# Kernel tuning notes

Measured on AMD Instinct MI355X. Metric: run time of the kernel, lower is better.

The kernel has to match this reference:

```python
import jax, jax.numpy as jnp
import numpy as np

EPS = 1e-5


def setup_inputs() -> dict:
    key = jax.random.key(0)
    ks = jax.random.split(key, 14)
    N, C, H, W, D = 2048, 512, 4, 4, 64
    inp = {
        "x": jax.random.normal(ks[0], (N, C, H, W), jnp.float32),
        "W123": jax.random.normal(ks[1], (3, D, C), jnp.float32) * 0.05,
        "b123": jax.random.normal(ks[2], (3, D), jnp.float32) * 0.05,
        "g123": jax.random.uniform(ks[3], (3, D), jnp.float32, 0.5, 1.5),
        "be123": jax.random.normal(ks[4], (3, D), jnp.float32) * 0.05,
        "m123": jax.random.normal(ks[5], (3, D), jnp.float32) * 0.05,
        "v123": jax.random.uniform(ks[6], (3, D), jnp.float32, 0.5, 1.5),
        "W4": jax.random.normal(ks[7], (C, D), jnp.float32) * 0.05,
        "b4": jax.random.normal(ks[8], (C,), jnp.float32) * 0.05,
        "g4": jax.random.uniform(ks[9], (C,), jnp.float32, 0.5, 1.5),
        "be4": jax.random.normal(ks[10], (C,), jnp.float32) * 0.05,
        "m4": jax.random.normal(ks[11], (C,), jnp.float32) * 0.05,
        "v4": jax.random.uniform(ks[12], (C,), jnp.float32, 0.5, 1.5),
    }
    return inp


def reference(x, W123, b123, g123, be123, m123, v123, W4, b4, g4, be4, m4, v4):
    N, C, H, W = x.shape
    D = W123.shape[1]
    # three parallel 1x1 stride-2 conv branches == strided slice + channel GEMM
    xs = x[:, :, ::2, ::2]                                 # (N, C, H/2, W/2)
    proj = jnp.einsum('nchw,koc->knohw', xs, W123)         # (3, N, D, H/2, W/2)
    bcast = lambda p: p[:, None, :, None, None]
    bn = (proj + bcast(b123) - bcast(m123)) * (bcast(g123) / jnp.sqrt(bcast(v123) + EPS)) + bcast(be123)
    act = jax.nn.relu(bn)                                  # (3, N, D, h, w)
    L = act.shape[-2] * act.shape[-1]
    q = act[0].reshape(N, D, L).transpose(0, 2, 1)         # (N, L, D)
    k = act[1].reshape(N, D, L)                            # (N, D, L)
    v = act[2].reshape(N, D, L).transpose(0, 2, 1)         # (N, L, D)
    attn = jax.nn.softmax(jnp.einsum('nld,ndm->nlm', q, k), axis=2)  # (N, L, L)
    att = jnp.einsum('nlm,nmd->nld', attn, v).transpose(0, 2, 1)     # (N, D, L)
    att = att.reshape(N, D, W, -1)                         # (N, D, W, L//W)
    # conv2: 1x1 conv D->C + BN (no ReLU)
    out2 = jnp.einsum('ndhw,cd->nchw', att, W4) + b4[None, :, None, None]
    cb = lambda p: p[None, :, None, None]
    bn2 = (out2 - cb(m4)) * (cb(g4) / jnp.sqrt(cb(v4) + EPS)) + cb(be4)
    return x + bn2                                         # broadcasts (N,C,4,1) -> (N,C,4,4)
```

## Files before the change

### kernel.cpp

```cpp
#include <hip/hip_runtime.h>
#include <hip/hip_bf16.h>
#include <math.h>

#define EPS 1e-5f

typedef __attribute__((ext_vector_type(8))) short bf8_t;
typedef __attribute__((ext_vector_type(4))) float f4_t;

static __device__ __forceinline__ unsigned short f2b(float f) {
    __hip_bfloat16 h = __float2bfloat16(f);
    return *reinterpret_cast<unsigned short*>(&h);
}


__global__ __launch_bounds__(256) void k0_prep(
    const float* __restrict__ W123, const float* __restrict__ W4,
    const float* __restrict__ b123, const float* __restrict__ g123,
    const float* __restrict__ be123, const float* __restrict__ m123, const float* __restrict__ v123,
    const float* __restrict__ b4, const float* __restrict__ g4,
    const float* __restrict__ be4, const float* __restrict__ m4, const float* __restrict__ v4,
    unsigned short* __restrict__ w1b, unsigned short* __restrict__ w4b,
    float* __restrict__ bn1s, float* __restrict__ bn1h,
    float* __restrict__ bn2s, float* __restrict__ bn2h)
{
    const int bid = blockIdx.x, tid = threadIdx.x;
    if (bid == 64) {
        if (tid < 192) {
            float s = g123[tid] * rsqrtf(v123[tid] + EPS);
            bn1s[tid] = s;
            bn1h[tid] = be123[tid] + (b123[tid] - m123[tid]) * s;
        }
        for (int c = tid; c < 512; c += 256) {
            float s = g4[c] * rsqrtf(v4[c] + EPS);
            bn2s[c] = s;
            bn2h[c] = be4[c] + (b4[c] - m4[c]) * s;
        }
        return;
    }
    const int f = bid * 256 + tid;
    const float* src;
    unsigned short* dst;
    if (f < 12288) {
        int mt = f >> 10, ks = (f >> 6) & 15, lane = f & 63;
        int row = mt * 16 + (lane & 15);
        int k0  = ks * 32 + ((lane >> 4) << 3);
        src = W123 + row * 512 + k0;
        dst = w1b + f * 8;
    } else {
        int f2 = f - 12288;
        int mt = f2 >> 7, ks = (f2 >> 6) & 1, lane = f2 & 63;
        int row = mt * 16 + (lane & 15);
        int k0  = ks * 32 + ((lane >> 4) << 3);
        src = W4 + row * 64 + k0;
        dst = w4b + f2 * 8;
    }
    float4 a = *(const float4*)src;
    float4 b = *(const float4*)(src + 4);
    union { unsigned short u[8]; uint4 v; } o;
    o.u[0]=f2b(a.x); o.u[1]=f2b(a.y); o.u[2]=f2b(a.z); o.u[3]=f2b(a.w);
    o.u[4]=f2b(b.x); o.u[5]=f2b(b.y); o.u[6]=f2b(b.z); o.u[7]=f2b(b.w);
    *(uint4*)dst = o.v;
}

__global__ __launch_bounds__(256) void k1_mfma(
    const float* __restrict__ x,
    const unsigned short* __restrict__ w1b,
    const unsigned short* __restrict__ w4b,
    const float* __restrict__ bn1s, const float* __restrict__ bn1h,
    const float* __restrict__ bn2s, const float* __restrict__ bn2h,
    float* __restrict__ out)
{
    __shared__ unsigned short Bxs[16][536];
    __shared__ float actL[192][17];
    __shared__ float smx[4][17];
    __shared__ unsigned short B2[16][72];

    const int tid = threadIdx.x;
    const int lane = tid & 63, w = tid >> 6;
    const int n0 = blockIdx.x * 4;

    #pragma unroll
    for (int it = 0; it < 8; ++it) {
        int i = it * 256 + tid;
        int s = i >> 9, c = i & 511;
        const float* xp = x + (size_t)(n0 + s) * 8192 + c * 16;
        float4 a = *(const float4*)xp;
        float4 b = *(const float4*)(xp + 8);
        Bxs[s * 4 + 0][c] = f2b(a.x);
        Bxs[s * 4 + 1][c] = f2b(a.z);
        Bxs[s * 4 + 2][c] = f2b(b.x);
        Bxs[s * 4 + 3][c] = f2b(b.z);
    }
    __syncthreads();

    {
        f4_t acc[3] = {};
        const bf8_t* Af = (const bf8_t*)w1b;
        const int col = lane & 15, kg = (lane >> 4) << 3;
        for (int ks = 0; ks < 16; ++ks) {
            bf8_t bf = *(const bf8_t*)&Bxs[col][ks * 32 + kg];
            #pragma unroll
            for (int mi = 0; mi < 3; ++mi) {
                int mt = w * 3 + mi;
                bf8_t af = Af[(mt * 16 + ks) * 64 + lane];
                acc[mi] = __builtin_amdgcn_mfma_f32_16x16x32_bf16(af, bf, acc[mi], 0, 0, 0);
            }
        }
        #pragma unroll
        for (int mi = 0; mi < 3; ++mi) {
            int rbase = (w * 3 + mi) * 16 + ((lane >> 4) << 2);
            #pragma unroll
            for (int r = 0; r < 4; ++r) {
                int row = rbase + r;
                float v = acc[mi][r] * bn1s[row] + bn1h[row];
                actL[row][col] = fmaxf(v, 0.f);
            }
        }
    }
    __syncthreads();

    if (tid < 128) {
        int s = tid >> 5, l = (tid >> 3) & 3, m = (tid >> 1) & 3, dg = tid & 1;
        float part = 0.f;
        #pragma unroll 8
        for (int k = 0; k < 32; ++k) {
            int d = dg * 32 + k;
            part += actL[d][s * 4 + l] * actL[64 + d][s * 4 + m];
        }
        part += __shfl_xor(part, 1);
        if (dg == 0) smx[s][l * 4 + m] = part;
    }
    __syncthreads();

    if (tid < 16) {
        int s = tid >> 2, l = tid & 3;
        float s0 = smx[s][l*4+0], s1 = smx[s][l*4+1], s2 = smx[s][l*4+2], s3 = smx[s][l*4+3];
        float mx = fmaxf(fmaxf(s0, s1), fmaxf(s2, s3));
        float e0 = expf(s0-mx), e1 = expf(s1-mx), e2 = expf(s2-mx), e3 = expf(s3-mx);
        float inv = 1.f / (e0 + e1 + e2 + e3);
        smx[s][l*4+0] = e0*inv; smx[s][l*4+1] = e1*inv;
        smx[s][l*4+2] = e2*inv; smx[s][l*4+3] = e3*inv;
    }
    __syncthreads();

    if (tid < 128) {
        int s = tid >> 5, l = (tid >> 3) & 3, d0 = (tid & 7) * 8;
        float p0 = smx[s][l*4+0], p1 = smx[s][l*4+1], p2 = smx[s][l*4+2], p3 = smx[s][l*4+3];
        #pragma unroll
        for (int j = 0; j < 8; ++j) {
            int d = d0 + j;
            float sum = p0 * actL[128+d][s*4+0] + p1 * actL[128+d][s*4+1]
                      + p2 * actL[128+d][s*4+2] + p3 * actL[128+d][s*4+3];
            B2[s * 4 + l][d] = f2b(sum);
        }
    }
    __syncthreads();

    {
        const bf8_t* A2f = (const bf8_t*)w4b;
        const int col = lane & 15, kg = (lane >> 4) << 3;
        f4_t acc2[8] = {};
        #pragma unroll
        for (int ks = 0; ks < 2; ++ks) {
            bf8_t bf = *(const bf8_t*)&B2[col][ks * 32 + kg];
            #pragma unroll
            for (int mi = 0; mi < 8; ++mi) {
                int mt = w * 8 + mi;
                bf8_t af = A2f[(mt * 2 + ks) * 64 + lane];
                acc2[mi] = __builtin_amdgcn_mfma_f32_16x16x32_bf16(af, bf, acc2[mi], 0, 0, 0);
            }
        }
        const int s = col >> 2, l = col & 3;
        const float* xn = x + (size_t)(n0 + s) * 8192 + l * 4;
        float* on = out + (size_t)(n0 + s) * 8192 + l * 4;
        #pragma unroll
        for (int mi = 0; mi < 8; ++mi) {
            int cbase = (w * 8 + mi) * 16 + ((lane >> 4) << 2);
            #pragma unroll
            for (int r = 0; r < 4; ++r) {
                int c = cbase + r;
                float b = acc2[mi][r] * bn2s[c] + bn2h[c];
                float4 xv = *(const float4*)(xn + c * 16);
                *(float4*)(on + c * 16) = make_float4(xv.x + b, xv.y + b, xv.z + b, xv.w + b);
            }
        }
    }
}

extern "C" void kernel_launch(void* const* d_in, const int* in_sizes, int n_in,
                              void* d_out, int out_size, void* d_ws, size_t ws_size,
                              hipStream_t stream) {
    const float* x     = (const float*)d_in[0];
    const float* W123  = (const float*)d_in[1];
    const float* b123  = (const float*)d_in[2];
    const float* g123  = (const float*)d_in[3];
    const float* be123 = (const float*)d_in[4];
    const float* m123  = (const float*)d_in[5];
    const float* v123  = (const float*)d_in[6];
    const float* W4    = (const float*)d_in[7];
    const float* b4    = (const float*)d_in[8];
    const float* g4    = (const float*)d_in[9];
    const float* be4   = (const float*)d_in[10];
    const float* m4    = (const float*)d_in[11];
    const float* v4    = (const float*)d_in[12];
    float* outp = (float*)d_out;

    char* ws = (char*)d_ws;
    unsigned short* w1b = (unsigned short*)ws;
    unsigned short* w4b = (unsigned short*)(ws + 196608);
    float* bn1s = (float*)(ws + 262144);
    float* bn1h = (float*)(ws + 262912);
    float* bn2s = (float*)(ws + 263680);
    float* bn2h = (float*)(ws + 265728);

    k0_prep<<<65, 256, 0, stream>>>(W123, W4, b123, g123, be123, m123, v123,
                                    b4, g4, be4, m4, v4,
                                    w1b, w4b, bn1s, bn1h, bn2s, bn2h);
    k1_mfma<<<512, 256, 0, stream>>>(x, w1b, w4b, bn1s, bn1h, bn2s, bn2h, outp);
}
```

Baseline: 152.6 us.

## Halve samples per block and stage epilogue through LDS for coalesced stores

Each block now handles 2 samples instead of 4, doubling the grid to 1024 blocks for better CU occupancy and latency hiding. The 16-column MFMA tiles are half-filled, with columns duplicated via col&7, so half the matrix-core work is wasted. The final residual add now writes the BN2 results to a shared transpose buffer and then streams x and out with contiguous float4 accesses per thread, replacing the scattered 16-float-stride epilogue. Each block also re-reads the weights for fewer samples, which raises total weight traffic.

```diff
diff --git a/kernel.cpp b/kernel.cpp
--- a/kernel.cpp
+++ b/kernel.cpp
@@ -70,17 +70,18 @@
     const float* __restrict__ bn2s, const float* __restrict__ bn2h,
     float* __restrict__ out)
 {
-    __shared__ unsigned short Bxs[16][536];
-    __shared__ float actL[192][17];
-    __shared__ float smx[4][17];
-    __shared__ unsigned short B2[16][72];
+    __shared__ unsigned short Bxs[8][536];
+    __shared__ float actL[192][9];
+    __shared__ float smx[2][17];
+    __shared__ unsigned short B2[8][72];
+    __shared__ float C2T[8][524];
 
     const int tid = threadIdx.x;
     const int lane = tid & 63, w = tid >> 6;
-    const int n0 = blockIdx.x * 4;
+    const int n0 = blockIdx.x * 2;
 
     #pragma unroll
-    for (int it = 0; it < 8; ++it) {
+    for (int it = 0; it < 4; ++it) {
         int i = it * 256 + tid;
         int s = i >> 9, c = i & 511;
         const float* xp = x + (size_t)(n0 + s) * 8192 + c * 16;
@@ -98,7 +99,7 @@
         const bf8_t* Af = (const bf8_t*)w1b;
         const int col = lane & 15, kg = (lane >> 4) << 3;
         for (int ks = 0; ks < 16; ++ks) {
-            bf8_t bf = *(const bf8_t*)&Bxs[col][ks * 32 + kg];
+            bf8_t bf = *(const bf8_t*)&Bxs[col & 7][ks * 32 + kg];
             #pragma unroll
             for (int mi = 0; mi < 3; ++mi) {
                 int mt = w * 3 + mi;
@@ -106,20 +107,22 @@
                 acc[mi] = __builtin_amdgcn_mfma_f32_16x16x32_bf16(af, bf, acc[mi], 0, 0, 0);
             }
         }
-        #pragma unroll
-        for (int mi = 0; mi < 3; ++mi) {
-            int rbase = (w * 3 + mi) * 16 + ((lane >> 4) << 2);
-            #pragma unroll
-            for (int r = 0; r < 4; ++r) {
-                int row = rbase + r;
-                float v = acc[mi][r] * bn1s[row] + bn1h[row];
-                actL[row][col] = fmaxf(v, 0.f);
-            }
-        }
-    }
-    __syncthreads();
-
-    if (tid < 128) {
+        if (col < 8) {
+            #pragma unroll
+            for (int mi = 0; mi < 3; ++mi) {
+                int rbase = (w * 3 + mi) * 16 + ((lane >> 4) << 2);
+                #pragma unroll
+                for (int r = 0; r < 4; ++r) {
+                    int row = rbase + r;
+                    float v = acc[mi][r] * bn1s[row] + bn1h[row];
+                    actL[row][col] = fmaxf(v, 0.f);
+                }
+            }
+        }
+    }
+    __syncthreads();
+
+    if (tid < 64) {
         int s = tid >> 5, l = (tid >> 3) & 3, m = (tid >> 1) & 3, dg = tid & 1;
         float part = 0.f;
         #pragma unroll 8
@@ -132,7 +135,7 @@
     }
     __syncthreads();
 
-    if (tid < 16) {
+    if (tid < 8) {
         int s = tid >> 2, l = tid & 3;
         float s0 = smx[s][l*4+0], s1 = smx[s][l*4+1], s2 = smx[s][l*4+2], s3 = smx[s][l*4+3];
         float mx = fmaxf(fmaxf(s0, s1), fmaxf(s2, s3));
@@ -143,7 +146,7 @@
     }
     __syncthreads();
 
-    if (tid < 128) {
+    if (tid < 64) {
         int s = tid >> 5, l = (tid >> 3) & 3, d0 = (tid & 7) * 8;
         float p0 = smx[s][l*4+0], p1 = smx[s][l*4+1], p2 = smx[s][l*4+2], p3 = smx[s][l*4+3];
         #pragma unroll
@@ -162,7 +165,7 @@
         f4_t acc2[8] = {};
         #pragma unroll
         for (int ks = 0; ks < 2; ++ks) {
-            bf8_t bf = *(const bf8_t*)&B2[col][ks * 32 + kg];
+            bf8_t bf = *(const bf8_t*)&B2[col & 7][ks * 32 + kg];
             #pragma unroll
             for (int mi = 0; mi < 8; ++mi) {
                 int mt = w * 8 + mi;
@@ -170,20 +173,32 @@
                 acc2[mi] = __builtin_amdgcn_mfma_f32_16x16x32_bf16(af, bf, acc2[mi], 0, 0, 0);
             }
         }
-        const int s = col >> 2, l = col & 3;
-        const float* xn = x + (size_t)(n0 + s) * 8192 + l * 4;
-        float* on = out + (size_t)(n0 + s) * 8192 + l * 4;
-        #pragma unroll
-        for (int mi = 0; mi < 8; ++mi) {
-            int cbase = (w * 8 + mi) * 16 + ((lane >> 4) << 2);
-            #pragma unroll
-            for (int r = 0; r < 4; ++r) {
-                int c = cbase + r;
-                float b = acc2[mi][r] * bn2s[c] + bn2h[c];
-                float4 xv = *(const float4*)(xn + c * 16);
-                *(float4*)(on + c * 16) = make_float4(xv.x + b, xv.y + b, xv.z + b, xv.w + b);
-            }
-        }
+        if (col < 8) {
+            #pragma unroll
+            for (int mi = 0; mi < 8; ++mi) {
+                int cbase = (w * 8 + mi) * 16 + ((lane >> 4) << 2);
+                #pragma unroll
+                for (int r = 0; r < 4; ++r) {
+                    int c = cbase + r;
+                    C2T[col][c] = acc2[mi][r] * bn2s[c] + bn2h[c];
+                }
+            }
+        }
+    }
+    __syncthreads();
+
+    #pragma unroll
+    for (int it = 0; it < 8; ++it) {
+        int j = it * 256 + tid;
+        int s = j >> 10, rem = j & 1023, c = rem >> 1, half = rem & 1;
+        const float* xp = x + (size_t)(n0 + s) * 8192 + c * 16 + half * 8;
+        float* op = out + (size_t)(n0 + s) * 8192 + c * 16 + half * 8;
+        float b0 = C2T[s * 4 + half * 2 + 0][c];
+        float b1 = C2T[s * 4 + half * 2 + 1][c];
+        float4 x0 = *(const float4*)xp;
+        float4 x1 = *(const float4*)(xp + 4);
+        *(float4*)op       = make_float4(x0.x + b0, x0.y + b0, x0.z + b0, x0.w + b0);
+        *(float4*)(op + 4) = make_float4(x1.x + b1, x1.y + b1, x1.z + b1, x1.w + b1);
     }
 }
 
@@ -216,5 +231,5 @@
     k0_prep<<<65, 256, 0, stream>>>(W123, W4, b123, g123, be123, m123, v123,
                                     b4, g4, be4, m4, v4,
                                     w1b, w4b, bn1s, bn1h, bn2s, bn2h);
-    k1_mfma<<<512, 256, 0, stream>>>(x, w1b, w4b, bn1s, bn1h, bn2s, bn2h, outp);
-}
+    k1_mfma<<<1024, 256, 0, stream>>>(x, w1b, w4b, bn1s, bn1h, bn2s, bn2h, outp);
+}
```

Result: no change. 152.1 us (-0.4%).

## Process one sample per block with shrunk aliased LDS and coalesced x I/O

Applied to the files above, without the earlier changes.

Switches from four samples per block to one sample per block, quadrupling the grid, and overlays the LDS buffers to cut shared memory so more blocks fit per CU. Input x is now read with fully coalesced float4 loads. The residual output is staged through LDS and written coalesced. In exchange, the 16-wide MFMA column dimension is mostly wasted and each block re-reads the full bf16 weight tiles, raising total weight traffic fourfold.

```diff
diff --git a/kernel.cpp b/kernel.cpp
--- a/kernel.cpp
+++ b/kernel.cpp
@@ -62,7 +62,7 @@
     *(uint4*)dst = o.v;
 }
 
-__global__ __launch_bounds__(256) void k1_mfma(
+__global__ __launch_bounds__(256, 8) void k1_mfma(
     const float* __restrict__ x,
     const unsigned short* __restrict__ w1b,
     const unsigned short* __restrict__ w4b,
@@ -70,35 +70,41 @@
     const float* __restrict__ bn2s, const float* __restrict__ bn2h,
     float* __restrict__ out)
 {
-    __shared__ unsigned short Bxs[16][536];
-    __shared__ float actL[192][17];
-    __shared__ float smx[4][17];
-    __shared__ unsigned short B2[16][72];
+    __shared__ __align__(16) char U[8768];
+    __shared__ float smx[20];
+
+    unsigned short* Bxs  = (unsigned short*)&U[0];
+    float*          actL = (float*)&U[4160];
+    unsigned short* B2   = (unsigned short*)&U[0];
+    float*          bn2L = (float*)&U[576];
 
     const int tid = threadIdx.x;
     const int lane = tid & 63, w = tid >> 6;
-    const int n0 = blockIdx.x * 4;
+    const int n = blockIdx.x;
+    const float4* x4 = (const float4*)(x + (size_t)n * 8192);
+    float4* o4 = (float4*)(out + (size_t)n * 8192);
 
     #pragma unroll
-    for (int it = 0; it < 8; ++it) {
-        int i = it * 256 + tid;
-        int s = i >> 9, c = i & 511;
-        const float* xp = x + (size_t)(n0 + s) * 8192 + c * 16;
-        float4 a = *(const float4*)xp;
-        float4 b = *(const float4*)(xp + 8);
-        Bxs[s * 4 + 0][c] = f2b(a.x);
-        Bxs[s * 4 + 1][c] = f2b(a.z);
-        Bxs[s * 4 + 2][c] = f2b(b.x);
-        Bxs[s * 4 + 3][c] = f2b(b.z);
+    for (int k = 0; k < 8; ++k) {
+        int f = tid + k * 256;
+        float4 v = x4[f];
+        int c = f >> 2, j = f & 3;
+        if (j == 0) {
+            Bxs[0 * 520 + c] = f2b(v.x);
+            Bxs[1 * 520 + c] = f2b(v.z);
+        } else if (j == 2) {
+            Bxs[2 * 520 + c] = f2b(v.x);
+            Bxs[3 * 520 + c] = f2b(v.z);
+        }
     }
     __syncthreads();
 
     {
         f4_t acc[3] = {};
         const bf8_t* Af = (const bf8_t*)w1b;
-        const int col = lane & 15, kg = (lane >> 4) << 3;
+        const int col = lane & 15, kb = (lane >> 4) << 3;
         for (int ks = 0; ks < 16; ++ks) {
-            bf8_t bf = *(const bf8_t*)&Bxs[col][ks * 32 + kg];
+            bf8_t bf = *(const bf8_t*)&Bxs[(col & 3) * 520 + ks * 32 + kb];
             #pragma unroll
             for (int mi = 0; mi < 3; ++mi) {
                 int mt = w * 3 + mi;
@@ -106,63 +112,65 @@
                 acc[mi] = __builtin_amdgcn_mfma_f32_16x16x32_bf16(af, bf, acc[mi], 0, 0, 0);
             }
         }
-        #pragma unroll
-        for (int mi = 0; mi < 3; ++mi) {
-            int rbase = (w * 3 + mi) * 16 + ((lane >> 4) << 2);
-            #pragma unroll
-            for (int r = 0; r < 4; ++r) {
-                int row = rbase + r;
-                float v = acc[mi][r] * bn1s[row] + bn1h[row];
-                actL[row][col] = fmaxf(v, 0.f);
-            }
-        }
-    }
-    __syncthreads();
-
-    if (tid < 128) {
-        int s = tid >> 5, l = (tid >> 3) & 3, m = (tid >> 1) & 3, dg = tid & 1;
+        if (col < 4) {
+            #pragma unroll
+            for (int mi = 0; mi < 3; ++mi) {
+                int rbase = (w * 3 + mi) * 16 + ((lane >> 4) << 2);
+                #pragma unroll
+                for (int r = 0; r < 4; ++r) {
+                    int row = rbase + r;
+                    float v = acc[mi][r] * bn1s[row] + bn1h[row];
+                    actL[row * 5 + col] = fmaxf(v, 0.f);
+                }
+            }
+        }
+    }
+    __syncthreads();
+
+    if (tid < 32) {
+        int l = (tid >> 3) & 3, m = (tid >> 1) & 3, dg = tid & 1;
         float part = 0.f;
         #pragma unroll 8
-        for (int k = 0; k < 32; ++k) {
-            int d = dg * 32 + k;
-            part += actL[d][s * 4 + l] * actL[64 + d][s * 4 + m];
+        for (int kk = 0; kk < 32; ++kk) {
+            int d = dg * 32 + kk;
+            part += actL[d * 5 + l] * actL[(64 + d) * 5 + m];
         }
         part += __shfl_xor(part, 1);
-        if (dg == 0) smx[s][l * 4 + m] = part;
-    }
-    __syncthreads();
-
-    if (tid < 16) {
-        int s = tid >> 2, l = tid & 3;
-        float s0 = smx[s][l*4+0], s1 = smx[s][l*4+1], s2 = smx[s][l*4+2], s3 = smx[s][l*4+3];
+        if (dg == 0) smx[l * 4 + m] = part;
+    }
+    __syncthreads();
+
+    if (tid < 4) {
+        int l = tid;
+        float s0 = smx[l*4+0], s1 = smx[l*4+1], s2 = smx[l*4+2], s3 = smx[l*4+3];
         float mx = fmaxf(fmaxf(s0, s1), fmaxf(s2, s3));
         float e0 = expf(s0-mx), e1 = expf(s1-mx), e2 = expf(s2-mx), e3 = expf(s3-mx);
         float inv = 1.f / (e0 + e1 + e2 + e3);
-        smx[s][l*4+0] = e0*inv; smx[s][l*4+1] = e1*inv;
-        smx[s][l*4+2] = e2*inv; smx[s][l*4+3] = e3*inv;
-    }
-    __syncthreads();
-
-    if (tid < 128) {
-        int s = tid >> 5, l = (tid >> 3) & 3, d0 = (tid & 7) * 8;
-        float p0 = smx[s][l*4+0], p1 = smx[s][l*4+1], p2 = smx[s][l*4+2], p3 = smx[s][l*4+3];
+        smx[l*4+0] = e0*inv; smx[l*4+1] = e1*inv;
+        smx[l*4+2] = e2*inv; smx[l*4+3] = e3*inv;
+    }
+    __syncthreads();
+
+    if (tid < 32) {
+        int l = tid >> 3, d0 = (tid & 7) * 8;
+        float p0 = smx[l*4+0], p1 = smx[l*4+1], p2 = smx[l*4+2], p3 = smx[l*4+3];
         #pragma unroll
         for (int j = 0; j < 8; ++j) {
             int d = d0 + j;
-            float sum = p0 * actL[128+d][s*4+0] + p1 * actL[128+d][s*4+1]
-                      + p2 * actL[128+d][s*4+2] + p3 * actL[128+d][s*4+3];
-            B2[s * 4 + l][d] = f2b(sum);
+            float sum = p0 * actL[(128+d)*5 + 0] + p1 * actL[(128+d)*5 + 1]
+                      + p2 * actL[(128+d)*5 + 2] + p3 * actL[(128+d)*5 + 3];
+            B2[l * 72 + d] = f2b(sum);
         }
     }
     __syncthreads();
 
     {
         const bf8_t* A2f = (const bf8_t*)w4b;
-        const int col = lane & 15, kg = (lane >> 4) << 3;
+        const int col = lane & 15, kb = (lane >> 4) << 3;
         f4_t acc2[8] = {};
         #pragma unroll
         for (int ks = 0; ks < 2; ++ks) {
-            bf8_t bf = *(const bf8_t*)&B2[col][ks * 32 + kg];
+            bf8_t bf = *(const bf8_t*)&B2[(col & 3) * 72 + ks * 32 + kb];
             #pragma unroll
             for (int mi = 0; mi < 8; ++mi) {
                 int mt = w * 8 + mi;
@@ -170,20 +178,27 @@
                 acc2[mi] = __builtin_amdgcn_mfma_f32_16x16x32_bf16(af, bf, acc2[mi], 0, 0, 0);
             }
         }
-        const int s = col >> 2, l = col & 3;
-        const float* xn = x + (size_t)(n0 + s) * 8192 + l * 4;
-        float* on = out + (size_t)(n0 + s) * 8192 + l * 4;
-        #pragma unroll
-        for (int mi = 0; mi < 8; ++mi) {
-            int cbase = (w * 8 + mi) * 16 + ((lane >> 4) << 2);
-            #pragma unroll
-            for (int r = 0; r < 4; ++r) {
-                int c = cbase + r;
-                float b = acc2[mi][r] * bn2s[c] + bn2h[c];
-                float4 xv = *(const float4*)(xn + c * 16);
-                *(float4*)(on + c * 16) = make_float4(xv.x + b, xv.y + b, xv.z + b, xv.w + b);
-            }
-        }
+        if (col < 4) {
+            #pragma unroll
+            for (int mi = 0; mi < 8; ++mi) {
+                int cbase = (w * 8 + mi) * 16 + ((lane >> 4) << 2);
+                #pragma unroll
+                for (int r = 0; r < 4; ++r) {
+                    int c = cbase + r;
+                    bn2L[c * 4 + col] = acc2[mi][r] * bn2s[c] + bn2h[c];
+                }
+            }
+        }
+    }
+    __syncthreads();
+
+    #pragma unroll
+    for (int k = 0; k < 8; ++k) {
+        int f = tid + k * 256;
+        int c = f >> 2, j = f & 3;
+        float b = bn2L[c * 4 + j];
+        float4 v = x4[f];
+        o4[f] = make_float4(v.x + b, v.y + b, v.z + b, v.w + b);
     }
 }
 
@@ -216,5 +231,5 @@
     k0_prep<<<65, 256, 0, stream>>>(W123, W4, b123, g123, be123, m123, v123,
                                     b4, g4, be4, m4, v4,
                                     w1b, w4b, bn1s, bn1h, bn2s, bn2h);
-    k1_mfma<<<512, 256, 0, stream>>>(x, w1b, w4b, bn1s, bn1h, bn2s, bn2h, outp);
-}
+    k1_mfma<<<2048, 256, 0, stream>>>(x, w1b, w4b, bn1s, bn1h, bn2s, bn2h, outp);
+}
```

New measurement: 188.1 us. 23.2% more time.

## Split fused kernel into attention and output kernels with coalesced epilogue

Applied to the files above, without the earlier changes.

Splits the single fused kernel in two. The first computes the attention output and writes it to a bf16 workspace; the second, launched one block per sample, applies the output projection and residual add, staging BN results in shared memory so x is read and out is written as fully coalesced float4 streams. The first kernel also hoists its global x loads ahead of the LDS stores and software-prefetches the weight fragments two k-steps ahead in the MFMA loop. The cost is an extra launch, a workspace round trip, and a second full read of x, in exchange for better memory access patterns and higher parallelism in the output stage.

```diff
diff --git a/kernel.cpp b/kernel.cpp
--- a/kernel.cpp
+++ b/kernel.cpp
@@ -62,34 +62,36 @@
     *(uint4*)dst = o.v;
 }
 
-__global__ __launch_bounds__(256) void k1_mfma(
+__global__ __launch_bounds__(256) void k1_att(
     const float* __restrict__ x,
     const unsigned short* __restrict__ w1b,
-    const unsigned short* __restrict__ w4b,
     const float* __restrict__ bn1s, const float* __restrict__ bn1h,
-    const float* __restrict__ bn2s, const float* __restrict__ bn2h,
-    float* __restrict__ out)
+    unsigned short* __restrict__ attg)
 {
     __shared__ unsigned short Bxs[16][536];
     __shared__ float actL[192][17];
     __shared__ float smx[4][17];
-    __shared__ unsigned short B2[16][72];
 
     const int tid = threadIdx.x;
     const int lane = tid & 63, w = tid >> 6;
     const int n0 = blockIdx.x * 4;
 
+    float4 xa[8], xb[8];
+    #pragma unroll
+    for (int it = 0; it < 8; ++it) {
+        int i = it * 256 + tid;
+        const float* xp = x + (size_t)(n0 + (i >> 9)) * 8192 + (i & 511) * 16;
+        xa[it] = *(const float4*)xp;
+        xb[it] = *(const float4*)(xp + 8);
+    }
     #pragma unroll
     for (int it = 0; it < 8; ++it) {
         int i = it * 256 + tid;
         int s = i >> 9, c = i & 511;
-        const float* xp = x + (size_t)(n0 + s) * 8192 + c * 16;
-        float4 a = *(const float4*)xp;
-        float4 b = *(const float4*)(xp + 8);
-        Bxs[s * 4 + 0][c] = f2b(a.x);
-        Bxs[s * 4 + 1][c] = f2b(a.z);
-        Bxs[s * 4 + 2][c] = f2b(b.x);
-        Bxs[s * 4 + 3][c] = f2b(b.z);
+        Bxs[s * 4 + 0][c] = f2b(xa[it].x);
+        Bxs[s * 4 + 1][c] = f2b(xa[it].z);
+        Bxs[s * 4 + 2][c] = f2b(xb[it].x);
+        Bxs[s * 4 + 3][c] = f2b(xb[it].z);
     }
     __syncthreads();
 
@@ -97,14 +99,23 @@
         f4_t acc[3] = {};
         const bf8_t* Af = (const bf8_t*)w1b;
         const int col = lane & 15, kg = (lane >> 4) << 3;
+        bf8_t afp[3][3];
+        #pragma unroll
+        for (int mi = 0; mi < 3; ++mi) {
+            afp[0][mi] = Af[((w * 3 + mi) * 16 + 0) * 64 + lane];
+            afp[1][mi] = Af[((w * 3 + mi) * 16 + 1) * 64 + lane];
+        }
+        #pragma unroll
         for (int ks = 0; ks < 16; ++ks) {
+            if (ks < 14) {
+                #pragma unroll
+                for (int mi = 0; mi < 3; ++mi)
+                    afp[(ks + 2) % 3][mi] = Af[((w * 3 + mi) * 16 + ks + 2) * 64 + lane];
+            }
             bf8_t bf = *(const bf8_t*)&Bxs[col][ks * 32 + kg];
             #pragma unroll
-            for (int mi = 0; mi < 3; ++mi) {
-                int mt = w * 3 + mi;
-                bf8_t af = Af[(mt * 16 + ks) * 64 + lane];
-                acc[mi] = __builtin_amdgcn_mfma_f32_16x16x32_bf16(af, bf, acc[mi], 0, 0, 0);
-            }
+            for (int mi = 0; mi < 3; ++mi)
+                acc[mi] = __builtin_amdgcn_mfma_f32_16x16x32_bf16(afp[ks % 3][mi], bf, acc[mi], 0, 0, 0);
         }
         #pragma unroll
         for (int mi = 0; mi < 3; ++mi) {
@@ -146,23 +157,52 @@
     if (tid < 128) {
         int s = tid >> 5, l = (tid >> 3) & 3, d0 = (tid & 7) * 8;
         float p0 = smx[s][l*4+0], p1 = smx[s][l*4+1], p2 = smx[s][l*4+2], p3 = smx[s][l*4+3];
+        union { unsigned short u[8]; uint4 v; } o;
         #pragma unroll
         for (int j = 0; j < 8; ++j) {
             int d = d0 + j;
             float sum = p0 * actL[128+d][s*4+0] + p1 * actL[128+d][s*4+1]
                       + p2 * actL[128+d][s*4+2] + p3 * actL[128+d][s*4+3];
-            B2[s * 4 + l][d] = f2b(sum);
-        }
+            o.u[j] = f2b(sum);
+        }
+        *(uint4*)&attg[(size_t)(n0 + s) * 256 + l * 64 + d0] = o.v;
+    }
+}
+
+__global__ __launch_bounds__(256) void k2_out(
+    const float* __restrict__ x,
+    const unsigned short* __restrict__ attg,
+    const unsigned short* __restrict__ w4b,
+    const float* __restrict__ bn2s, const float* __restrict__ bn2h,
+    float* __restrict__ out)
+{
+    __shared__ unsigned short B2[4][72];
+    __shared__ float bn2L[2048];
+
+    const int tid = threadIdx.x;
+    const int lane = tid & 63, w = tid >> 6;
+    const int n = blockIdx.x;
+    const float4* x4 = (const float4*)(x + (size_t)n * 8192);
+    float4* o4 = (float4*)(out + (size_t)n * 8192);
+
+    float4 xr[8];
+    #pragma unroll
+    for (int k = 0; k < 8; ++k) xr[k] = x4[tid + k * 256];
+
+    if (tid < 32) {
+        uint4 v = *(const uint4*)&attg[(size_t)n * 256 + tid * 8];
+        int l = tid >> 3, d0 = (tid & 7) * 8;
+        *(uint4*)&B2[l][d0] = v;
     }
     __syncthreads();
 
     {
         const bf8_t* A2f = (const bf8_t*)w4b;
-        const int col = lane & 15, kg = (lane >> 4) << 3;
+        const int col = lane & 15, kb = (lane >> 4) << 3;
         f4_t acc2[8] = {};
         #pragma unroll
         for (int ks = 0; ks < 2; ++ks) {
-            bf8_t bf = *(const bf8_t*)&B2[col][ks * 32 + kg];
+            bf8_t bf = *(const bf8_t*)&B2[col & 3][ks * 32 + kb];
             #pragma unroll
             for (int mi = 0; mi < 8; ++mi) {
                 int mt = w * 8 + mi;
@@ -170,20 +210,25 @@
                 acc2[mi] = __builtin_amdgcn_mfma_f32_16x16x32_bf16(af, bf, acc2[mi], 0, 0, 0);
             }
         }
-        const int s = col >> 2, l = col & 3;
-        const float* xn = x + (size_t)(n0 + s) * 8192 + l * 4;
-        float* on = out + (size_t)(n0 + s) * 8192 + l * 4;
-        #pragma unroll
-        for (int mi = 0; mi < 8; ++mi) {
-            int cbase = (w * 8 + mi) * 16 + ((lane >> 4) << 2);
-            #pragma unroll
-            for (int r = 0; r < 4; ++r) {
-                int c = cbase + r;
-                float b = acc2[mi][r] * bn2s[c] + bn2h[c];
-                float4 xv = *(const float4*)(xn + c * 16);
-                *(float4*)(on + c * 16) = make_float4(xv.x + b, xv.y + b, xv.z + b, xv.w + b);
-            }
-        }
+        if (col < 4) {
+            #pragma unroll
+            for (int mi = 0; mi < 8; ++mi) {
+                int cbase = (w * 8 + mi) * 16 + ((lane >> 4) << 2);
+                #pragma unroll
+                for (int r = 0; r < 4; ++r) {
+                    int c = cbase + r;
+                    bn2L[c * 4 + col] = acc2[mi][r] * bn2s[c] + bn2h[c];
+                }
+            }
+        }
+    }
+    __syncthreads();
+
+    #pragma unroll
+    for (int k = 0; k < 8; ++k) {
+        int f = tid + k * 256;
+        float b = bn2L[f];
+        o4[f] = make_float4(xr[k].x + b, xr[k].y + b, xr[k].z + b, xr[k].w + b);
     }
 }
 
@@ -212,9 +257,11 @@
     float* bn1h = (float*)(ws + 262912);
     float* bn2s = (float*)(ws + 263680);
     float* bn2h = (float*)(ws + 265728);
+    unsigned short* attg = (unsigned short*)(ws + 524288);
 
     k0_prep<<<65, 256, 0, stream>>>(W123, W4, b123, g123, be123, m123, v123,
                                     b4, g4, be4, m4, v4,
                                     w1b, w4b, bn1s, bn1h, bn2s, bn2h);
-    k1_mfma<<<512, 256, 0, stream>>>(x, w1b, w4b, bn1s, bn1h, bn2s, bn2h, outp);
-}
+    k1_att<<<512, 256, 0, stream>>>(x, w1b, bn1s, bn1h, attg);
+    k2_out<<<2048, 256, 0, stream>>>(x, attg, w4b, bn2s, bn2h, outp);
+}
```

After: 154.8 us. No clear change (+1.4%).
